# Kernel tuning notes

Hardware: AMD Instinct MI355X
Metric: run time of the kernel (lower is better)

## Reference

```python
import jax, jax.numpy as jnp
import numpy as np

PI = 3.141592653
MAXV = 8          # max vertices of the intersection of two convex quads
N_BOXES = 1024
IOU_THR = 0.1


def limit_period(val):
    return val - jnp.floor(val / (2.0 * PI) + 0.5) * (2.0 * PI)


def cross2(a, b):
    return a[..., 0] * b[..., 1] - a[..., 1] * b[..., 0]


def rect_corners(box):
    # box: [7] = x,y,z,dx,dy,dz,yaw -> [4,2] BEV corners, CCW order
    x, y, dx, dy, ang = box[0], box[1], box[3], box[4], box[6]
    local = jnp.array([[0.5, 0.5], [-0.5, 0.5], [-0.5, -0.5], [0.5, -0.5]],
                      dtype=box.dtype) * jnp.stack([dx, dy])
    c, s = jnp.cos(ang), jnp.sin(ang)
    rot = jnp.array([[c, -s], [s, c]])
    return local @ rot.T + jnp.stack([x, y])


def poly_area(verts, n):
    # shoelace over first n vertices of padded [MAXV,2] polygon
    idx = jnp.arange(MAXV)
    nxt = verts[jnp.where(idx == n - 1, 0, idx + 1)]
    valid = idx < n
    return 0.5 * jnp.abs(jnp.sum(jnp.where(valid, cross2(verts, nxt), 0.0)))


def bev_inter_area(box_a, box_b):
    # Sutherland-Hodgman: clip quad A against the 4 half-planes of quad B.
    pa = rect_corners(box_a)
    pb = rect_corners(box_b)
    verts0 = jnp.zeros((MAXV, 2), pa.dtype).at[:4].set(pa)
    edges = jnp.stack([pb, jnp.roll(pb, -1, axis=0)], axis=1)  # [4,2,2]

    def clip(carry, e):
        v, n = carry
        a, b = e[0], e[1]
        idx = jnp.arange(MAXV)
        prev = v[jnp.where(idx == 0, n - 1, idx - 1)]
        d = b - a
        sp = cross2(d, v - a)     # signed side of current vertex
        sq = cross2(d, prev - a)  # signed side of previous vertex
        in_p, in_q = sp >= 0, sq >= 0
        den = sq - sp
        den = jnp.where(jnp.abs(den) < 1e-9, 1e-9, den)
        t = sq / den
        inter = prev + t[:, None] * (v - prev)
        live = idx < n
        emit_i = live & (in_p != in_q)   # crossing -> emit intersection
        emit_p = live & in_p             # inside -> emit vertex
        pts = jnp.stack([inter, v], axis=1).reshape(2 * MAXV, 2)
        msk = jnp.stack([emit_i, emit_p], axis=1).reshape(2 * MAXV)
        pos = jnp.where(msk, jnp.cumsum(msk) - 1, MAXV)  # compact; OOB dropped
        nv = jnp.zeros((MAXV, 2), v.dtype).at[pos].set(pts, mode='drop')
        return (nv, jnp.sum(msk).astype(jnp.int32)), None

    (v, n), _ = jax.lax.scan(clip, (verts0, jnp.int32(4)), edges)
    return jnp.where(n >= 3, poly_area(v, n), 0.0)


def iou3d_pair(a, b):
    inter_bev = bev_inter_area(a, b)
    h = jnp.maximum(jnp.minimum(a[2] + a[5] * 0.5, b[2] + b[5] * 0.5)
                    - jnp.maximum(a[2] - a[5] * 0.5, b[2] - b[5] * 0.5), 0.0)
    inter = inter_bev * h
    va = a[3] * a[4] * a[5]
    vb = b[3] * b[4] * b[5]
    return inter / jnp.maximum(va + vb - inter, 1e-6)


def clustering(ious):
    # exact translation of the sequential while-loop: repeatedly take the
    # first unassigned box, assign everything with iou > 0.1 to a new cluster
    # id (later clusters may overwrite earlier assignments, as in the source).
    N = ious.shape[0]

    def body(i, carry):
        ci, cid = carry
        has_zero = jnp.any(ci == 0)
        cur = jnp.argmax(ci == 0)
        m = ious[cur] > IOU_THR
        ci = jnp.where(has_zero & m, cid, ci)
        return (ci, cid + has_zero.astype(jnp.int32))

    ci, _ = jax.lax.fori_loop(0, N, body, (jnp.zeros(N, jnp.int32), jnp.int32(1)))
    return ci


def fuse_cluster(m, boxes, scores):
    # m: bool[N] membership mask for one cluster
    s = jnp.where(m, scores, 0.0)
    ssum = jnp.sum(s)
    dirs = boxes[:, 6]
    ref = dirs[jnp.argmax(s)]                    # direction of max-score member
    diff = jnp.abs(dirs - ref)
    diff = jnp.where(diff > PI, 2.0 * PI - diff, diff)
    gt = diff > PI / 2
    sc_gt = jnp.sum(jnp.where(m & gt, scores, 0.0))
    sc_le = ssum - sc_gt
    flip_gt = sc_gt <= sc_le                     # flip minority orientation group
    add = jnp.where(flip_gt, gt, ~gt)
    d2 = limit_period(dirs + PI * add.astype(boxes.dtype))
    sn = s / jnp.where(ssum > 0, ssum, 1.0)
    theta = jnp.arctan2(jnp.sum(jnp.sin(d2) * sn), jnp.sum(jnp.cos(d2) * sn))
    center = jnp.sum(boxes[:, :6] * sn[:, None], axis=0)
    box_f = jnp.concatenate([center, theta[None]])
    # score fusion: sum_i s_(i)^(i+1) over descending-sorted member scores
    s_sorted = jnp.sort(s)[::-1]
    powers = jnp.arange(1, s.shape[0] + 1, dtype=s.dtype)
    s_f = jnp.minimum(jnp.sum(s_sorted ** powers), 1.0)
    return box_f, s_f


def setup_inputs() -> dict:
    key = jax.random.key(0)
    k = jax.random.split(key, 6)
    xy = jax.random.uniform(k[0], (N_BOXES, 2), minval=0.0, maxval=140.0)
    z = jax.random.uniform(k[1], (N_BOXES, 1), minval=-1.0, maxval=1.0)
    dxy = jax.random.uniform(k[2], (N_BOXES, 2), minval=1.5, maxval=4.5)
    dz = jax.random.uniform(k[3], (N_BOXES, 1), minval=1.0, maxval=2.0)
    yaw = jax.random.uniform(k[4], (N_BOXES, 1), minval=-PI, maxval=PI)
    det_boxes = jnp.concatenate([xy, z, dxy, dz, yaw], axis=1)
    det_scores = jax.random.uniform(k[5], (N_BOXES,), minval=0.01, maxval=1.0)
    return {"det_boxes": det_boxes, "det_scores": det_scores}


def reference(det_boxes, det_scores):
    N = det_boxes.shape[0]
    boxes = det_boxes.at[:, 6].set(limit_period(det_boxes[:, 6]))
    ious = jax.vmap(lambda a: jax.vmap(lambda b: iou3d_pair(a, b))(boxes))(boxes)
    ci = clustering(ious)                               # int32[N], ids in 1..N
    masks = ci[None, :] == jnp.arange(1, N + 1)[:, None]  # [N clusters, N boxes]
    boxes_f, scores_f = jax.vmap(fuse_cluster, in_axes=(0, None, None))(masks, boxes, det_scores)
    valid = jnp.any(masks, axis=1)
    boxes_f = jnp.where(valid[:, None], boxes_f, 0.0)
    scores_f = jnp.where(valid, scores_f, 0.0)
    return boxes_f, scores_f, valid
```

## Files before the change

### kernel.cpp

```cpp
#include <hip/hip_runtime.h>

#define PI_F 3.141592653f
#define NB 1024
#define NW 16
#define IOU_THR_F 0.1f
#define NBLK 256
#define MB_MAGIC 0x33333333u
#define MC_MAGIC 0x5EEDF00Du

__device__ __forceinline__ float limit_period_f(float v) {
    return v - floorf(v / (2.0f * PI_F) + 0.5f) * (2.0f * PI_F);
}

__device__ __forceinline__ int widx(int r, int w) {
    return (r << 4) | (w ^ (r & 15));
}

__device__ __forceinline__ float iou_pair(const float* __restrict__ boxes, int i, int j,
                                          float* vxs, float* vys, int tid)
{
    const float xi  = boxes[i*7+0], yi  = boxes[i*7+1], zi  = boxes[i*7+2];
    const float dxi = boxes[i*7+3], dyi = boxes[i*7+4], dzi = boxes[i*7+5];
    const float aang = limit_period_f(boxes[i*7+6]);
    const float xj  = boxes[j*7+0], yj  = boxes[j*7+1], zj  = boxes[j*7+2];
    const float dxj = boxes[j*7+3], dyj = boxes[j*7+4], dzj = boxes[j*7+5];
    const float bang = limit_period_f(boxes[j*7+6]);

    float ca, sa, cb, sb;
    sincosf(aang, &sa, &ca);
    sincosf(bang, &sb, &cb);

    {
        const float hx = 0.5f*dxi, hy = 0.5f*dyi;
        const float lxs[4] = { hx, -hx, -hx, hx };
        const float lys[4] = { hy, hy, -hy, -hy };
        #pragma unroll
        for (int k = 0; k < 4; ++k) {
            vxs[(0*8+k)*256 + tid] = lxs[k]*ca - lys[k]*sa + xi;
            vys[(0*8+k)*256 + tid] = lxs[k]*sa + lys[k]*ca + yi;
        }
    }
    float pbx[4], pby[4];
    {
        const float hx = 0.5f*dxj, hy = 0.5f*dyj;
        const float lxs[4] = { hx, -hx, -hx, hx };
        const float lys[4] = { hy, hy, -hy, -hy };
        #pragma unroll
        for (int k = 0; k < 4; ++k) {
            pbx[k] = lxs[k]*cb - lys[k]*sb + xj;
            pby[k] = lxs[k]*sb + lys[k]*cb + yj;
        }
    }

    int n = 4;
    int cur = 0;
    #pragma unroll
    for (int e4 = 0; e4 < 4; ++e4) {
        const float eax = pbx[e4], eay = pby[e4];
        const float ebx2 = pbx[(e4+1)&3], eby2 = pby[(e4+1)&3];
        const float dx = ebx2 - eax, dy = eby2 - eay;
        int m = 0;
        if (n > 0) {
            int pidx = n - 1; if (pidx > 7) pidx = 7;
            float px = vxs[(cur*8+pidx)*256 + tid];
            float py = vys[(cur*8+pidx)*256 + tid];
            float sq = dx*(py - eay) - dy*(px - eax);
            #pragma unroll
            for (int k = 0; k < 8; ++k) {
                if (k < n) {
                    const float cx = vxs[(cur*8+k)*256 + tid];
                    const float cy = vys[(cur*8+k)*256 + tid];
                    const float sp = dx*(cy - eay) - dy*(cx - eax);
                    const bool in_p = (sp >= 0.0f);
                    const bool in_q = (sq >= 0.0f);
                    if (in_p != in_q) {
                        float den = sq - sp;
                        den = (fabsf(den) < 1e-9f) ? 1e-9f : den;
                        const float t = sq / den;
                        if (m < 8) {
                            vxs[((cur^1)*8+m)*256 + tid] = px + t*(cx - px);
                            vys[((cur^1)*8+m)*256 + tid] = py + t*(cy - py);
                        }
                        ++m;
                    }
                    if (in_p) {
                        if (m < 8) {
                            vxs[((cur^1)*8+m)*256 + tid] = cx;
                            vys[((cur^1)*8+m)*256 + tid] = cy;
                        }
                        ++m;
                    }
                    px = cx; py = cy; sq = sp;
                }
            }
        }
        n = m;
        cur ^= 1;
    }

    float area = 0.0f;
    if (n >= 3) {
        float s = 0.0f;
        const float x0 = vxs[(cur*8+0)*256 + tid];
        const float y0 = vys[(cur*8+0)*256 + tid];
        #pragma unroll
        for (int k = 0; k < 8; ++k) {
            if (k < n) {
                float nx, ny;
                if (k == n - 1) { nx = x0; ny = y0; }
                else {
                    int nk = k + 1; if (nk > 7) nk = 7;
                    nx = vxs[(cur*8+nk)*256 + tid]; ny = vys[(cur*8+nk)*256 + tid];
                }
                s += vxs[(cur*8+k)*256 + tid]*ny - vys[(cur*8+k)*256 + tid]*nx;
            }
        }
        area = 0.5f * fabsf(s);
    }

    const float zh = fminf(zi + dzi*0.5f, zj + dzj*0.5f);
    const float zl = fmaxf(zi - dzi*0.5f, zj - dzj*0.5f);
    const float h = fmaxf(zh - zl, 0.0f);
    const float inter = area * h;
    const float va = dxi*dyi*dzi;
    const float vb = dxj*dyj*dzj;
    return inter / fmaxf(va + vb - inter, 1e-6f);
}

__global__ __launch_bounds__(256) void fused_kernel(
    const float* __restrict__ boxes,
    const float* __restrict__ scores,
    float* __restrict__ out,
    unsigned long long* __restrict__ maskT,
    unsigned int* __restrict__ wm_g,
    unsigned long long* __restrict__ ci_pack,
    unsigned int* __restrict__ slotB,
    unsigned int* __restrict__ flagC)
{
    extern __shared__ char smem[];
    __shared__ int candN;
    const int tid = threadIdx.x;
    const int b = blockIdx.x;
    const int lane = tid & 63;
    const int wave = tid >> 6;

    float* vxs = (float*)smem;
    float* vys = (float*)(smem + 16384);
    unsigned long long (*rowW)[NW] = (unsigned long long (*)[NW])(smem + 32768);
    unsigned int* candL = (unsigned int*)(smem + 33280);

    if (tid == 0) candN = 0;
    __syncthreads();

    for (int rr = 0; rr < 4; ++rr) {
        const int j = b * 4 + rr;
        const float xj  = boxes[j*7+0], yj  = boxes[j*7+1];
        const float dxj = boxes[j*7+3], dyj = boxes[j*7+4];
        const float rb2 = 0.25f*(dxj*dxj + dyj*dyj);
        #pragma unroll
        for (int q = 0; q < 4; ++q) {
            const int i = q*256 + tid;
            const float xi  = boxes[i*7+0], yi  = boxes[i*7+1];
            const float dxi = boxes[i*7+3], dyi = boxes[i*7+4];
            const float ddx = xi - xj, ddy = yi - yj;
            const float d2 = ddx*ddx + ddy*ddy;
            const float ra2 = 0.25f*(dxi*dxi + dyi*dyi);
            const bool cand = d2 <= 2.0f*(ra2 + rb2);

            const unsigned long long bal = __ballot(cand);
            const int w = q*4 + wave;
            if (lane == 0) rowW[rr][w] = bal;

            unsigned long long keep = bal;
            if ((j >> 6) == w) keep &= ~(1ull << (j & 63));
            int basep = 0;
            if (lane == 0 && keep) basep = atomicAdd(&candN, (int)__popcll(keep));
            basep = __shfl(basep, 0);
            if ((keep >> lane) & 1ull) {
                const int pos = basep + (int)__popcll(keep & ((1ull << lane) - 1ull));
                candL[pos] = ((unsigned)rr << 10) | (unsigned)i;
            }
        }
    }
    __syncthreads();
    const int nc = candN;

    for (int e = tid; e < nc; e += 256) {
        const unsigned int ent = candL[e];
        const int rr = (int)(ent >> 10);
        const int i  = (int)(ent & 1023u);
        const int j  = b * 4 + rr;
        const float iou = iou_pair(boxes, i, j, vxs, vys, tid);
        if (!(iou > IOU_THR_F)) {
            unsigned int* hw = (unsigned int*)&rowW[rr][i >> 6];
            atomicAnd(&hw[(i >> 5) & 1], ~(1u << (i & 31)));
        }
    }
    __syncthreads();

    if (tid < 64) {
        const int rr = tid >> 4, w = tid & 15;
        const unsigned long long v = rowW[rr][w];
        const int j = b * 4 + rr;
        if (v != 0ull)
            __hip_atomic_store(&maskT[(size_t)j*NW + w], v,
                               __ATOMIC_RELAXED, __HIP_MEMORY_SCOPE_AGENT);
        const unsigned long long wb = __ballot(v != 0ull);
        if ((tid & 15) == 0)
            __hip_atomic_store(&wm_g[j], (unsigned int)((wb >> (16*rr)) & 0xFFFFull),
                               __ATOMIC_RELAXED, __HIP_MEMORY_SCOPE_AGENT);
    }
    __syncthreads();
    if (tid == 0) {
        asm volatile("s_waitcnt vmcnt(0)" ::: "memory");
        __hip_atomic_store(&slotB[b], MB_MAGIC, __ATOMIC_RELAXED, __HIP_MEMORY_SCOPE_AGENT);
    }

    if (b == 0) {
        unsigned long long* mat = (unsigned long long*)smem;
        unsigned short* wm = (unsigned short*)(smem + 131072);
        unsigned long long* seed_lds = (unsigned long long*)(smem + 133120);
        int* rankb = (int*)(smem + 133248);
        unsigned long long* packL = (unsigned long long*)(smem + 133312);

        if (tid < NW) { seed_lds[tid] = 0ull; rankb[tid] = 0; }

        while (__hip_atomic_load(&slotB[tid], __ATOMIC_RELAXED, __HIP_MEMORY_SCOPE_AGENT) != MB_MAGIC)
            __builtin_amdgcn_s_sleep(1);
        #pragma unroll
        for (int rr = 0; rr < 4; ++rr) {
            const int r = tid * 4 + rr;
            const unsigned int m16 =
                __hip_atomic_load(&wm_g[r], __ATOMIC_RELAXED, __HIP_MEMORY_SCOPE_AGENT) & 0xFFFFu;
            wm[r] = (unsigned short)m16;
            unsigned int t16 = m16;
            while (t16) {
                const int w = __ffs(t16) - 1;
                t16 &= t16 - 1;
                mat[widx(r, w)] =
                    __hip_atomic_load(&maskT[(size_t)r * NW + w],
                                      __ATOMIC_RELAXED, __HIP_MEMORY_SCOPE_AGENT);
            }
        }
        __syncthreads();

        if (tid < 64) {
            int base = 0;
            for (int c = 0; c < NW; ++c) {
                const int row = c * 64 + tid;
                unsigned int f = (unsigned int)wm[row];
                unsigned long long acc = 0ull, Dt = 0ull;
                while (f) {
                    const int w = __ffs(f) - 1;
                    f &= f - 1;
                    const unsigned long long v = mat[widx(row, w)];
                    acc |= v & seed_lds[w];
                    if (w == c) Dt = v;
                }
                const bool elig = (acc == 0ull);
                const unsigned long long E = __ballot(elig);
                const unsigned long long inlow = Dt & ((1ull << tid) - 1ull);

                unsigned long long S = E;
                #pragma unroll 1
                for (int it = 0; it < 64; ++it) {
                    const bool killed = (inlow & S) != 0ull;
                    const unsigned long long S2 = E & __ballot(!killed);
                    if (S2 == S) break;
                    S = S2;
                }

                if (tid == 0) { seed_lds[c] = S; rankb[c] = base; }
                base += (int)__popcll(S);
            }
        }
        __syncthreads();

        {
            unsigned long long pk = 0ull;
            #pragma unroll
            for (int rr = 0; rr < 4; ++rr) {
                const int r = tid * 4 + rr;
                unsigned int f = (unsigned int)wm[r];
                int best = -1;
                while (f) {
                    const int w = __ffs(f) - 1;
                    f &= f - 1;
                    const unsigned long long bits = mat[widx(r, w)] & seed_lds[w];
                    if (bits) best = (w << 6) | (63 - __clzll(bits));
                }
                int lbl = 0;
                if (best >= 0) {
                    const int w = best >> 6, pos = best & 63;
                    lbl = rankb[w] + (int)__popcll(seed_lds[w] & ((1ull << pos) - 1ull)) + 1;
                }
                pk |= (unsigned long long)(unsigned)lbl << (16 * rr);
            }
            packL[tid] = pk;
        }
        __syncthreads();

        if (tid < 64) {
            #pragma unroll
            for (int q = 0; q < 4; ++q)
                __hip_atomic_store(&ci_pack[tid + q*64], packL[tid + q*64],
                                   __ATOMIC_RELAXED, __HIP_MEMORY_SCOPE_AGENT);
        }
        if (tid == 0) {
            asm volatile("s_waitcnt vmcnt(0)" ::: "memory");
            __hip_atomic_store(flagC, MC_MAGIC, __ATOMIC_RELAXED, __HIP_MEMORY_SCOPE_AGENT);
        }
    } else {
        if (tid == 0) {
            while (__hip_atomic_load(flagC, __ATOMIC_RELAXED, __HIP_MEMORY_SCOPE_AGENT) != MC_MAGIC)
                __builtin_amdgcn_s_sleep(1);
        }
    }
    __syncthreads();

    {
        float* ms = (float*)smem + wave * 1024;
        int*   mi = (int*)(smem + 16384) + wave * 1024;
        const int target = b * 4 + wave + 1;
        const int ob = target - 1;

        unsigned int mymask = 0;
        #pragma unroll
        for (int k4 = 0; k4 < 4; ++k4) {
            const unsigned long long pw =
                __hip_atomic_load(&ci_pack[lane * 4 + k4],
                                  __ATOMIC_RELAXED, __HIP_MEMORY_SCOPE_AGENT);
            #pragma unroll
            for (int s = 0; s < 4; ++s)
                if (((pw >> (16*s)) & 0xFFFFull) == (unsigned long long)(unsigned)target)
                    mymask |= 1u << (k4*4 + s);
        }
        const bool anyv = (__ballot(mymask != 0) != 0ULL);

        float* outb = out + (size_t)ob * 7;
        float* outs = out + 7 * NB;
        float* outv = out + 8 * NB;

        if (!anyv) {
            if (lane == 0) {
                #pragma unroll
                for (int c = 0; c < 7; ++c) outb[c] = 0.0f;
                outs[ob] = 0.0f;
                outv[ob] = 0.0f;
            }
        } else {
            float ssum = 0.0f, smax = -1.0f;
            int sidx = 1 << 30;
            #pragma unroll
            for (int k = 0; k < 16; ++k) {
                if (mymask & (1u << k)) {
                    const int idx = lane * 16 + k;
                    const float s = scores[idx];
                    ssum += s;
                    if (s > smax || (s == smax && idx < sidx)) { smax = s; sidx = idx; }
                }
            }
            #pragma unroll
            for (int off = 32; off >= 1; off >>= 1) {
                ssum += __shfl_xor(ssum, off);
                const float om = __shfl_xor(smax, off);
                const int   oi = __shfl_xor(sidx, off);
                if (om > smax || (om == smax && oi < sidx)) { smax = om; sidx = oi; }
            }
            const float ref = limit_period_f(boxes[sidx * 7 + 6]);

            float sc_gt = 0.0f;
            #pragma unroll
            for (int k = 0; k < 16; ++k) {
                if (mymask & (1u << k)) {
                    const int idx = lane * 16 + k;
                    const float dir = limit_period_f(boxes[idx * 7 + 6]);
                    float diff = fabsf(dir - ref);
                    if (diff > PI_F) diff = 2.0f * PI_F - diff;
                    if (diff > PI_F * 0.5f) sc_gt += scores[idx];
                }
            }
            #pragma unroll
            for (int off = 32; off >= 1; off >>= 1) sc_gt += __shfl_xor(sc_gt, off);
            const bool flip_gt = (sc_gt <= (ssum - sc_gt));

            float acc[6] = {0,0,0,0,0,0};
            float ssin = 0.0f, scos = 0.0f;
            #pragma unroll
            for (int k = 0; k < 16; ++k) {
                if (mymask & (1u << k)) {
                    const int idx = lane * 16 + k;
                    const float s = scores[idx];
                    const float w = s / ssum;
                    const float dir = limit_period_f(boxes[idx * 7 + 6]);
                    float diff = fabsf(dir - ref);
                    if (diff > PI_F) diff = 2.0f * PI_F - diff;
                    const bool gt = (diff > PI_F * 0.5f);
                    const bool add = flip_gt ? gt : (!gt);
                    const float d2 = limit_period_f(dir + (add ? PI_F : 0.0f));
                    float sd, cd;
                    sincosf(d2, &sd, &cd);
                    ssin += sd * w;
                    scos += cd * w;
                    #pragma unroll
                    for (int c = 0; c < 6; ++c) acc[c] += boxes[idx * 7 + c] * w;
                }
            }
            #pragma unroll
            for (int off = 32; off >= 1; off >>= 1) {
                ssin += __shfl_xor(ssin, off);
                scos += __shfl_xor(scos, off);
                #pragma unroll
                for (int c = 0; c < 6; ++c) acc[c] += __shfl_xor(acc[c], off);
            }
            const float theta = atan2f(ssin, scos);

            const int cnt = __popc(mymask);
            int x = cnt;
            #pragma unroll
            for (int off = 1; off < 64; off <<= 1) {
                const int y = __shfl_up(x, off);
                if (lane >= off) x += y;
            }
            const int base = x - cnt;
            const int K = __shfl(x, 63);
            {
                int p = base;
                #pragma unroll
                for (int k = 0; k < 16; ++k) {
                    if (mymask & (1u << k)) {
                        const int idx = lane * 16 + k;
                        ms[p] = scores[idx];
                        mi[p] = idx;
                        ++p;
                    }
                }
            }
            float sf = 0.0f;
            for (int e = lane; e < K; e += 64) {
                const float v = ms[e];
                const int ix = mi[e];
                int rank = 0;
                for (int t = 0; t < K; ++t) {
                    const float u = ms[t];
                    if (u > v || (u == v && mi[t] < ix)) ++rank;
                }
                sf += powf(v, (float)(rank + 1));
            }
            #pragma unroll
            for (int off = 32; off >= 1; off >>= 1) sf += __shfl_xor(sf, off);
            sf = fminf(sf, 1.0f);

            if (lane == 0) {
                #pragma unroll
                for (int c = 0; c < 6; ++c) outb[c] = acc[c];
                outb[6] = theta;
                outs[ob] = sf;
                outv[ob] = 1.0f;
            }
        }
    }
}

extern "C" void kernel_launch(void* const* d_in, const int* in_sizes, int n_in,
                              void* d_out, int out_size, void* d_ws, size_t ws_size,
                              hipStream_t stream) {
    const float* boxes  = (const float*)d_in[0];
    const float* scores = (const float*)d_in[1];
    float* out = (float*)d_out;

    char* ws = (char*)d_ws;
    unsigned long long* maskT = (unsigned long long*)ws;
    unsigned int* wm_g = (unsigned int*)(ws + 131072);
    unsigned long long* ci_pack = (unsigned long long*)(ws + 135168);
    unsigned int* slotB = (unsigned int*)(ws + 137216);
    unsigned int* flagC = (unsigned int*)(ws + 138240);

    const size_t SMEM = 135360;
    (void)hipFuncSetAttribute((const void*)fused_kernel,
                              hipFuncAttributeMaxDynamicSharedMemorySize, (int)SMEM);
    fused_kernel<<<NBLK, 256, SMEM, stream>>>(
        boxes, scores, out, maskT, wm_g, ci_pack, slotB, flagC);
}
```

Before: 85.32 us.

## Spread completion flag, prefetch fuse inputs to LDS while waiting, drop word-mask array

Non-leader blocks now stage scores, wrapped yaw and transposed box fields into LDS while they wait for the clustering block, and then read those values during fusion instead of global memory. The single completion flag is replicated into 32 flags on separate cache lines so spinning blocks do not all poll one address, and the sleep interval is longer. The per-row nonzero word mask array is removed: every mask word is always stored, and the leader block loads all 16 words per row in one batch and derives the mask itself. Block 0 reads cluster labels from its own LDS. The cost is more global stores and loads of mask words in exchange for fewer dependent load round trips and less polling contention.

Measured after the change: 91.80 us. 7.6% more time.

```diff
diff --git a/kernel.cpp b/kernel.cpp
--- a/kernel.cpp
+++ b/kernel.cpp
@@ -132,10 +132,9 @@
     const float* __restrict__ scores,
     float* __restrict__ out,
     unsigned long long* __restrict__ maskT,
-    unsigned int* __restrict__ wm_g,
     unsigned long long* __restrict__ ci_pack,
     unsigned int* __restrict__ slotB,
-    unsigned int* __restrict__ flagC)
+    unsigned int* __restrict__ flagCv)
 {
     extern __shared__ char smem[];
     __shared__ int candN;
@@ -200,15 +199,8 @@
 
     if (tid < 64) {
         const int rr = tid >> 4, w = tid & 15;
-        const unsigned long long v = rowW[rr][w];
-        const int j = b * 4 + rr;
-        if (v != 0ull)
-            __hip_atomic_store(&maskT[(size_t)j*NW + w], v,
-                               __ATOMIC_RELAXED, __HIP_MEMORY_SCOPE_AGENT);
-        const unsigned long long wb = __ballot(v != 0ull);
-        if ((tid & 15) == 0)
-            __hip_atomic_store(&wm_g[j], (unsigned int)((wb >> (16*rr)) & 0xFFFFull),
-                               __ATOMIC_RELAXED, __HIP_MEMORY_SCOPE_AGENT);
+        __hip_atomic_store(&maskT[(size_t)(b*4+rr)*NW + w], rowW[rr][w],
+                           __ATOMIC_RELAXED, __HIP_MEMORY_SCOPE_AGENT);
     }
     __syncthreads();
     if (tid == 0) {
@@ -230,17 +222,17 @@
         #pragma unroll
         for (int rr = 0; rr < 4; ++rr) {
             const int r = tid * 4 + rr;
-            const unsigned int m16 =
-                __hip_atomic_load(&wm_g[r], __ATOMIC_RELAXED, __HIP_MEMORY_SCOPE_AGENT) & 0xFFFFu;
+            unsigned long long v[NW];
+            #pragma unroll
+            for (int w = 0; w < NW; ++w)
+                v[w] = __hip_atomic_load(&maskT[(size_t)r * NW + w],
+                                         __ATOMIC_RELAXED, __HIP_MEMORY_SCOPE_AGENT);
+            unsigned int m16 = 0;
+            #pragma unroll
+            for (int w = 0; w < NW; ++w) {
+                if (v[w] != 0ull) { m16 |= 1u << w; mat[widx(r, w)] = v[w]; }
+            }
             wm[r] = (unsigned short)m16;
-            unsigned int t16 = m16;
-            while (t16) {
-                const int w = __ffs(t16) - 1;
-                t16 &= t16 - 1;
-                mat[widx(r, w)] =
-                    __hip_atomic_load(&maskT[(size_t)r * NW + w],
-                                      __ATOMIC_RELAXED, __HIP_MEMORY_SCOPE_AGENT);
-            }
         }
         __syncthreads();
 
@@ -305,31 +297,47 @@
             for (int q = 0; q < 4; ++q)
                 __hip_atomic_store(&ci_pack[tid + q*64], packL[tid + q*64],
                                    __ATOMIC_RELAXED, __HIP_MEMORY_SCOPE_AGENT);
+            asm volatile("s_waitcnt vmcnt(0)" ::: "memory");
+            if (tid < 32)
+                __hip_atomic_store(&flagCv[tid * 32], MC_MAGIC,
+                                   __ATOMIC_RELAXED, __HIP_MEMORY_SCOPE_AGENT);
+        }
+    } else {
+        float* bx      = (float*)smem;
+        float* s_lds   = (float*)(smem + 24576);
+        float* dir_lds = (float*)(smem + 28672);
+        for (int i = tid; i < NB; i += 256) {
+            s_lds[i]   = scores[i];
+            dir_lds[i] = limit_period_f(boxes[i*7+6]);
+            #pragma unroll
+            for (int c = 0; c < 6; ++c) bx[c*NB + i] = boxes[i*7+c];
         }
         if (tid == 0) {
-            asm volatile("s_waitcnt vmcnt(0)" ::: "memory");
-            __hip_atomic_store(flagC, MC_MAGIC, __ATOMIC_RELAXED, __HIP_MEMORY_SCOPE_AGENT);
-        }
-    } else {
-        if (tid == 0) {
-            while (__hip_atomic_load(flagC, __ATOMIC_RELAXED, __HIP_MEMORY_SCOPE_AGENT) != MC_MAGIC)
-                __builtin_amdgcn_s_sleep(1);
+            while (__hip_atomic_load(&flagCv[(b & 31) * 32],
+                                     __ATOMIC_RELAXED, __HIP_MEMORY_SCOPE_AGENT) != MC_MAGIC)
+                __builtin_amdgcn_s_sleep(16);
         }
     }
     __syncthreads();
 
     {
-        float* ms = (float*)smem + wave * 1024;
-        int*   mi = (int*)(smem + 16384) + wave * 1024;
+        float* ms = (float*)(smem + 32768) + wave * 1024;
+        int*   mi = (int*)  (smem + 49152) + wave * 1024;
+        const bool uL = (b != 0);
+        const float* bx      = (const float*)smem;
+        const float* s_lds   = (const float*)(smem + 24576);
+        const float* dir_lds = (const float*)(smem + 28672);
+        const unsigned long long* packL = (const unsigned long long*)(smem + 133312);
         const int target = b * 4 + wave + 1;
         const int ob = target - 1;
 
         unsigned int mymask = 0;
         #pragma unroll
         for (int k4 = 0; k4 < 4; ++k4) {
-            const unsigned long long pw =
-                __hip_atomic_load(&ci_pack[lane * 4 + k4],
-                                  __ATOMIC_RELAXED, __HIP_MEMORY_SCOPE_AGENT);
+            const unsigned long long pw = uL
+                ? __hip_atomic_load(&ci_pack[lane * 4 + k4],
+                                    __ATOMIC_RELAXED, __HIP_MEMORY_SCOPE_AGENT)
+                : packL[lane * 4 + k4];
             #pragma unroll
             for (int s = 0; s < 4; ++s)
                 if (((pw >> (16*s)) & 0xFFFFull) == (unsigned long long)(unsigned)target)
@@ -355,7 +363,7 @@
             for (int k = 0; k < 16; ++k) {
                 if (mymask & (1u << k)) {
                     const int idx = lane * 16 + k;
-                    const float s = scores[idx];
+                    const float s = uL ? s_lds[idx] : scores[idx];
                     ssum += s;
                     if (s > smax || (s == smax && idx < sidx)) { smax = s; sidx = idx; }
                 }
@@ -367,17 +375,17 @@
                 const int   oi = __shfl_xor(sidx, off);
                 if (om > smax || (om == smax && oi < sidx)) { smax = om; sidx = oi; }
             }
-            const float ref = limit_period_f(boxes[sidx * 7 + 6]);
+            const float ref = uL ? dir_lds[sidx] : limit_period_f(boxes[sidx * 7 + 6]);
 
             float sc_gt = 0.0f;
             #pragma unroll
             for (int k = 0; k < 16; ++k) {
                 if (mymask & (1u << k)) {
                     const int idx = lane * 16 + k;
-                    const float dir = limit_period_f(boxes[idx * 7 + 6]);
+                    const float dir = uL ? dir_lds[idx] : limit_period_f(boxes[idx * 7 + 6]);
                     float diff = fabsf(dir - ref);
                     if (diff > PI_F) diff = 2.0f * PI_F - diff;
-                    if (diff > PI_F * 0.5f) sc_gt += scores[idx];
+                    if (diff > PI_F * 0.5f) sc_gt += (uL ? s_lds[idx] : scores[idx]);
                 }
             }
             #pragma unroll
@@ -390,9 +398,9 @@
             for (int k = 0; k < 16; ++k) {
                 if (mymask & (1u << k)) {
                     const int idx = lane * 16 + k;
-                    const float s = scores[idx];
+                    const float s = uL ? s_lds[idx] : scores[idx];
                     const float w = s / ssum;
-                    const float dir = limit_period_f(boxes[idx * 7 + 6]);
+                    const float dir = uL ? dir_lds[idx] : limit_period_f(boxes[idx * 7 + 6]);
                     float diff = fabsf(dir - ref);
                     if (diff > PI_F) diff = 2.0f * PI_F - diff;
                     const bool gt = (diff > PI_F * 0.5f);
@@ -403,7 +411,8 @@
                     ssin += sd * w;
                     scos += cd * w;
                     #pragma unroll
-                    for (int c = 0; c < 6; ++c) acc[c] += boxes[idx * 7 + c] * w;
+                    for (int c = 0; c < 6; ++c)
+                        acc[c] += (uL ? bx[c*NB + idx] : boxes[idx * 7 + c]) * w;
                 }
             }
             #pragma unroll
@@ -430,7 +439,7 @@
                 for (int k = 0; k < 16; ++k) {
                     if (mymask & (1u << k)) {
                         const int idx = lane * 16 + k;
-                        ms[p] = scores[idx];
+                        ms[p] = uL ? s_lds[idx] : scores[idx];
                         mi[p] = idx;
                         ++p;
                     }
@@ -471,14 +480,13 @@
 
     char* ws = (char*)d_ws;
     unsigned long long* maskT = (unsigned long long*)ws;
-    unsigned int* wm_g = (unsigned int*)(ws + 131072);
-    unsigned long long* ci_pack = (unsigned long long*)(ws + 135168);
-    unsigned int* slotB = (unsigned int*)(ws + 137216);
-    unsigned int* flagC = (unsigned int*)(ws + 138240);
+    unsigned long long* ci_pack = (unsigned long long*)(ws + 131072);
+    unsigned int* slotB = (unsigned int*)(ws + 133120);
+    unsigned int* flagCv = (unsigned int*)(ws + 134144);
 
     const size_t SMEM = 135360;
     (void)hipFuncSetAttribute((const void*)fused_kernel,
                               hipFuncAttributeMaxDynamicSharedMemorySize, (int)SMEM);
     fused_kernel<<<NBLK, 256, SMEM, stream>>>(
-        boxes, scores, out, maskT, wm_g, ci_pack, slotB, flagC);
+        boxes, scores, out, maskT, ci_pack, slotB, flagCv);
 }
```

## Replicate clustering in every block to remove the second grid-wide barrier

Applied to the files above, without the earlier changes.

Instead of block 0 computing cluster labels and publishing them through a global flag that all other blocks spin on, every block waits on the per-block slot flags, loads the full mask matrix into LDS and runs the greedy clustering itself. Labels are kept in LDS for the fusion stage. The full mask rows are now written unconditionally, which drops the sparse word bitmap, and the slot flags are padded to separate cache lines. This removes one serialized cross-block handoff. In exchange, every block does redundant clustering work and reads the whole 128KB matrix, which adds L2 traffic.

New measurement: 106.9 us. +25.3%, slower.

```diff
diff --git a/kernel.cpp b/kernel.cpp
--- a/kernel.cpp
+++ b/kernel.cpp
@@ -6,7 +6,6 @@
 #define IOU_THR_F 0.1f
 #define NBLK 256
 #define MB_MAGIC 0x33333333u
-#define MC_MAGIC 0x5EEDF00Du
 
 __device__ __forceinline__ float limit_period_f(float v) {
     return v - floorf(v / (2.0f * PI_F) + 0.5f) * (2.0f * PI_F);
@@ -132,10 +131,7 @@
     const float* __restrict__ scores,
     float* __restrict__ out,
     unsigned long long* __restrict__ maskT,
-    unsigned int* __restrict__ wm_g,
-    unsigned long long* __restrict__ ci_pack,
-    unsigned int* __restrict__ slotB,
-    unsigned int* __restrict__ flagC)
+    unsigned int* __restrict__ slotB)
 {
     extern __shared__ char smem[];
     __shared__ int candN;
@@ -199,122 +195,90 @@
     __syncthreads();
 
     if (tid < 64) {
-        const int rr = tid >> 4, w = tid & 15;
-        const unsigned long long v = rowW[rr][w];
-        const int j = b * 4 + rr;
-        if (v != 0ull)
-            __hip_atomic_store(&maskT[(size_t)j*NW + w], v,
-                               __ATOMIC_RELAXED, __HIP_MEMORY_SCOPE_AGENT);
-        const unsigned long long wb = __ballot(v != 0ull);
-        if ((tid & 15) == 0)
-            __hip_atomic_store(&wm_g[j], (unsigned int)((wb >> (16*rr)) & 0xFFFFull),
-                               __ATOMIC_RELAXED, __HIP_MEMORY_SCOPE_AGENT);
+        __hip_atomic_store(&maskT[(size_t)b*64 + tid], rowW[tid >> 4][tid & 15],
+                           __ATOMIC_RELAXED, __HIP_MEMORY_SCOPE_AGENT);
     }
     __syncthreads();
     if (tid == 0) {
         asm volatile("s_waitcnt vmcnt(0)" ::: "memory");
-        __hip_atomic_store(&slotB[b], MB_MAGIC, __ATOMIC_RELAXED, __HIP_MEMORY_SCOPE_AGENT);
-    }
-
-    if (b == 0) {
-        unsigned long long* mat = (unsigned long long*)smem;
-        unsigned short* wm = (unsigned short*)(smem + 131072);
-        unsigned long long* seed_lds = (unsigned long long*)(smem + 133120);
-        int* rankb = (int*)(smem + 133248);
-        unsigned long long* packL = (unsigned long long*)(smem + 133312);
-
-        if (tid < NW) { seed_lds[tid] = 0ull; rankb[tid] = 0; }
-
-        while (__hip_atomic_load(&slotB[tid], __ATOMIC_RELAXED, __HIP_MEMORY_SCOPE_AGENT) != MB_MAGIC)
-            __builtin_amdgcn_s_sleep(1);
-        #pragma unroll
-        for (int rr = 0; rr < 4; ++rr) {
-            const int r = tid * 4 + rr;
-            const unsigned int m16 =
-                __hip_atomic_load(&wm_g[r], __ATOMIC_RELAXED, __HIP_MEMORY_SCOPE_AGENT) & 0xFFFFu;
-            wm[r] = (unsigned short)m16;
-            unsigned int t16 = m16;
-            while (t16) {
-                const int w = __ffs(t16) - 1;
-                t16 &= t16 - 1;
-                mat[widx(r, w)] =
-                    __hip_atomic_load(&maskT[(size_t)r * NW + w],
-                                      __ATOMIC_RELAXED, __HIP_MEMORY_SCOPE_AGENT);
-            }
-        }
-        __syncthreads();
-
-        if (tid < 64) {
-            int base = 0;
-            for (int c = 0; c < NW; ++c) {
-                const int row = c * 64 + tid;
-                unsigned int f = (unsigned int)wm[row];
-                unsigned long long acc = 0ull, Dt = 0ull;
-                while (f) {
-                    const int w = __ffs(f) - 1;
-                    f &= f - 1;
-                    const unsigned long long v = mat[widx(row, w)];
-                    acc |= v & seed_lds[w];
-                    if (w == c) Dt = v;
-                }
-                const bool elig = (acc == 0ull);
-                const unsigned long long E = __ballot(elig);
-                const unsigned long long inlow = Dt & ((1ull << tid) - 1ull);
-
-                unsigned long long S = E;
-                #pragma unroll 1
-                for (int it = 0; it < 64; ++it) {
-                    const bool killed = (inlow & S) != 0ull;
-                    const unsigned long long S2 = E & __ballot(!killed);
-                    if (S2 == S) break;
-                    S = S2;
-                }
-
-                if (tid == 0) { seed_lds[c] = S; rankb[c] = base; }
-                base += (int)__popcll(S);
-            }
-        }
-        __syncthreads();
-
-        {
-            unsigned long long pk = 0ull;
-            #pragma unroll
-            for (int rr = 0; rr < 4; ++rr) {
-                const int r = tid * 4 + rr;
-                unsigned int f = (unsigned int)wm[r];
-                int best = -1;
-                while (f) {
-                    const int w = __ffs(f) - 1;
-                    f &= f - 1;
-                    const unsigned long long bits = mat[widx(r, w)] & seed_lds[w];
-                    if (bits) best = (w << 6) | (63 - __clzll(bits));
-                }
-                int lbl = 0;
-                if (best >= 0) {
-                    const int w = best >> 6, pos = best & 63;
-                    lbl = rankb[w] + (int)__popcll(seed_lds[w] & ((1ull << pos) - 1ull)) + 1;
-                }
-                pk |= (unsigned long long)(unsigned)lbl << (16 * rr);
-            }
-            packL[tid] = pk;
-        }
-        __syncthreads();
-
-        if (tid < 64) {
-            #pragma unroll
-            for (int q = 0; q < 4; ++q)
-                __hip_atomic_store(&ci_pack[tid + q*64], packL[tid + q*64],
-                                   __ATOMIC_RELAXED, __HIP_MEMORY_SCOPE_AGENT);
+        __hip_atomic_store(&slotB[b * 32], MB_MAGIC,
+                           __ATOMIC_RELAXED, __HIP_MEMORY_SCOPE_AGENT);
+    }
+
+    while (__hip_atomic_load(&slotB[tid * 32], __ATOMIC_RELAXED,
+                             __HIP_MEMORY_SCOPE_AGENT) != MB_MAGIC)
+        __builtin_amdgcn_s_sleep(2);
+    __syncthreads();
+
+    unsigned long long* mat = (unsigned long long*)smem;
+    unsigned long long* seed_lds = (unsigned long long*)(smem + 133120);
+    int* rankb_lds = (int*)(smem + 133248);
+    int* ci_lds = (int*)(smem + 133312);
+
+    #pragma unroll 8
+    for (int it = 0; it < 64; ++it) {
+        const int idx = it * 256 + tid;
+        const unsigned long long v =
+            __hip_atomic_load(&maskT[idx], __ATOMIC_RELAXED, __HIP_MEMORY_SCOPE_AGENT);
+        mat[widx(idx >> 4, idx & 15)] = v;
+    }
+    __syncthreads();
+
+    if (tid < 64) {
+        unsigned long long seed[NW];
+        int rkb[NW];
+        #pragma unroll
+        for (int w = 0; w < NW; ++w) { seed[w] = 0ull; rkb[w] = 0; }
+        int base = 0;
+
+        #pragma unroll
+        for (int c = 0; c < NW; ++c) {
+            const int row = c * 64 + tid;
+            unsigned long long acc = 0ull, Dt = 0ull;
+            #pragma unroll
+            for (int w = 0; w < NW; ++w) {
+                const unsigned long long v = mat[widx(row, w)];
+                if (w == c) Dt = v;
+                else if (w < c) acc |= v & seed[w];
+            }
+            const bool elig = (acc == 0ull);
+            const unsigned long long E = __ballot(elig);
+            const unsigned long long inlow = Dt & ((1ull << tid) - 1ull);
+
+            unsigned long long S = E;
+            #pragma unroll 1
+            for (int it = 0; it < 64; ++it) {
+                const bool killed = (inlow & S) != 0ull;
+                const unsigned long long S2 = E & __ballot(!killed);
+                if (S2 == S) break;
+                S = S2;
+            }
+            seed[c] = S;
+            rkb[c] = base;
+            base += (int)__popcll(S);
         }
         if (tid == 0) {
-            asm volatile("s_waitcnt vmcnt(0)" ::: "memory");
-            __hip_atomic_store(flagC, MC_MAGIC, __ATOMIC_RELAXED, __HIP_MEMORY_SCOPE_AGENT);
-        }
-    } else {
-        if (tid == 0) {
-            while (__hip_atomic_load(flagC, __ATOMIC_RELAXED, __HIP_MEMORY_SCOPE_AGENT) != MC_MAGIC)
-                __builtin_amdgcn_s_sleep(1);
-        }
+            #pragma unroll
+            for (int w = 0; w < NW; ++w) { seed_lds[w] = seed[w]; rankb_lds[w] = rkb[w]; }
+        }
+    }
+    __syncthreads();
+
+    #pragma unroll
+    for (int rr4 = 0; rr4 < 4; ++rr4) {
+        const int r = tid * 4 + rr4;
+        int best = -1;
+        #pragma unroll
+        for (int w = 0; w < NW; ++w) {
+            const unsigned long long bits = mat[widx(r, w)] & seed_lds[w];
+            if (bits) best = (w << 6) | (63 - __clzll(bits));
+        }
+        int lbl = 0;
+        if (best >= 0) {
+            const int w = best >> 6, pos = best & 63;
+            lbl = rankb_lds[w] + (int)__popcll(seed_lds[w] & ((1ull << pos) - 1ull)) + 1;
+        }
+        ci_lds[r] = lbl;
     }
     __syncthreads();
 
@@ -326,14 +290,8 @@
 
         unsigned int mymask = 0;
         #pragma unroll
-        for (int k4 = 0; k4 < 4; ++k4) {
-            const unsigned long long pw =
-                __hip_atomic_load(&ci_pack[lane * 4 + k4],
-                                  __ATOMIC_RELAXED, __HIP_MEMORY_SCOPE_AGENT);
-            #pragma unroll
-            for (int s = 0; s < 4; ++s)
-                if (((pw >> (16*s)) & 0xFFFFull) == (unsigned long long)(unsigned)target)
-                    mymask |= 1u << (k4*4 + s);
+        for (int k = 0; k < 16; ++k) {
+            if (ci_lds[lane * 16 + k] == target) mymask |= 1u << k;
         }
         const bool anyv = (__ballot(mymask != 0) != 0ULL);
 
@@ -471,14 +429,10 @@
 
     char* ws = (char*)d_ws;
     unsigned long long* maskT = (unsigned long long*)ws;
-    unsigned int* wm_g = (unsigned int*)(ws + 131072);
-    unsigned long long* ci_pack = (unsigned long long*)(ws + 135168);
-    unsigned int* slotB = (unsigned int*)(ws + 137216);
-    unsigned int* flagC = (unsigned int*)(ws + 138240);
-
-    const size_t SMEM = 135360;
+    unsigned int* slotB = (unsigned int*)(ws + 131072);
+
+    const size_t SMEM = 137408;
     (void)hipFuncSetAttribute((const void*)fused_kernel,
                               hipFuncAttributeMaxDynamicSharedMemorySize, (int)SMEM);
-    fused_kernel<<<NBLK, 256, SMEM, stream>>>(
-        boxes, scores, out, maskT, wm_g, ci_pack, slotB, flagC);
+    fused_kernel<<<NBLK, 256, SMEM, stream>>>(boxes, scores, out, maskT, slotB);
 }
```
